# Performance work log

Hardware: AMD Instinct MI355X
Metric: run time of the kernel (lower is better)

## Reference

```python
import jax, jax.numpy as jnp
import numpy as np

N, E, NNZ = 50000, 10000, 250000   # nodes, hyperedges, incidences
IN_CH, H, D = 128, 64, 6           # in_channels, MLP_hidden, stalk dim
EPS = 1e-5


def setup_inputs() -> dict:
    key = jax.random.key(0)
    ks = jax.random.split(key, 12)
    inp = {}
    inp["x"] = jax.random.normal(ks[0], (N, IN_CH), jnp.float32)
    inp["hyperedge_attr"] = jax.random.normal(ks[1], (E, IN_CH), jnp.float32)  # init_hedge='rand'
    inp["node_idx"] = jax.random.randint(ks[2], (NNZ,), 0, N)
    inp["edge_idx"] = jax.random.randint(ks[3], (NNZ,), 0, E)
    inp["node_types"] = jax.random.randint(ks[4], (N,), 0, 3)
    inp["hyperedge_types"] = jax.random.randint(ks[5], (E,), 0, 6)
    s = 1.0 / np.sqrt(IN_CH)
    inp["W_lin"] = jax.random.uniform(ks[6], (IN_CH, H * D), jnp.float32, -s, s)
    inp["b_lin"] = jnp.zeros((H * D,), jnp.float32)
    inp["ln_g"] = jnp.ones((2 * H,), jnp.float32)
    inp["ln_b"] = jnp.zeros((2 * H,), jnp.float32)
    s2 = 1.0 / np.sqrt(2 * H)
    inp["W_sheaf"] = jax.random.uniform(ks[7], (2 * H, D), jnp.float32, -s2, s2)
    inp["b_sheaf"] = jnp.zeros((D,), jnp.float32)
    s3 = 1.0 / np.sqrt(H)
    inp["W_conv0"] = jax.random.uniform(ks[8], (H, H), jnp.float32, -s3, s3)
    inp["b_conv0"] = jnp.zeros((H,), jnp.float32)
    inp["W_conv1"] = jax.random.uniform(ks[9], (H, H), jnp.float32, -s3, s3)
    inp["b_conv1"] = jnp.zeros((H,), jnp.float32)
    return inp


def _layernorm(x, g, b):
    mu = x.mean(-1, keepdims=True)
    var = ((x - mu) ** 2).mean(-1, keepdims=True)
    return (x - mu) * jax.lax.rsqrt(var + EPS) * g + b


def reference(x, hyperedge_attr, node_idx, edge_idx, node_types, hyperedge_types,
              W_lin, b_lin, ln_g, ln_b, W_sheaf, b_sheaf,
              W_conv0, b_conv0, W_conv1, b_conv1):
    # --- input projection + stalk reshape (self.lin) ---
    xs = (x @ W_lin + b_lin).reshape(N * D, H)              # [N*d, H]
    es = (hyperedge_attr @ W_lin + b_lin).reshape(E * D, H)  # [E*d, H]

    # --- SheafBuilderDiag (local_concat, sigmoid act) ---
    xa = xs.reshape(N, D, H).mean(1)   # [N, H] stalk-averaged node feats
    ea = es.reshape(E, D, H).mean(1)   # [E, H]
    feat = jnp.concatenate([xa[node_idx], ea[edge_idx]], axis=-1)  # [NNZ, 2H]
    alpha = jax.nn.sigmoid(_layernorm(feat, ln_g, ln_b) @ W_sheaf + b_sheaf)  # [NNZ, D]

    dr = jnp.arange(D)
    row_exp = (node_idx[:, None] * D + dr).reshape(-1)  # [NNZ*D] expanded node index
    col_exp = (edge_idx[:, None] * D + dr).reshape(-1)  # [NNZ*D] expanded hyperedge index
    a = alpha.reshape(-1)                               # [NNZ*D]

    # --- degree_norm: D^-1 (nodes) and B^-1 (hyperedges) from incidence counts ---
    ones = jnp.ones_like(a)
    Dn = jax.ops.segment_sum(ones, row_exp, num_segments=N * D)
    Dinv = jnp.where(Dn > 0, 1.0 / Dn, 0.0)
    Bn = jax.ops.segment_sum(ones, col_exp, num_segments=E * D)
    Binv = jnp.where(Bn > 0, 1.0 / Bn, 0.0)

    def conv(xin, W, bias):
        # HyperDiffusionDiagSheafConv: out = xW - D^-1 H^T B^-1 H (xW) + bias
        xl = xin @ W
        m = Binv[:, None] * jax.ops.segment_sum(a[:, None] * xl[row_exp], col_exp, num_segments=E * D)
        agg = Dinv[:, None] * jax.ops.segment_sum(a[:, None] * m[col_exp], row_exp, num_segments=N * D)
        return xl - agg + bias

    h1 = jax.nn.elu(conv(xs, W_conv0, b_conv0))   # dropout inactive (eval)
    h2 = conv(h1, W_conv1, b_conv1)
    return jax.nn.elu(h2.reshape(N, H * D))
```

## Files before the change

### kernel.cpp

```cpp
#include <hip/hip_runtime.h>
#include <hip/hip_bf16.h>

#define N_NODES 50000
#define N_EDGES 10000
#define NNZV    250000
#define IN_CH   128
#define HDIM    64
#define DSTALK  6
#define HD      384
#define NROWS   (N_NODES * DSTALK)
#define EROWS   (N_EDGES * DSTALK)

__global__ __launch_bounds__(256) void k_weff(
    const float* __restrict__ W_lin, const float* __restrict__ W0,
    float* __restrict__ W0eff) {
  int idx = blockIdx.x * blockDim.x + threadIdx.x;
  if (idx >= IN_CH * HD) return;
  int k = idx / HD, j = idx - k * HD;
  int r = j >> 6, h = j & 63;
  float s = 0.f;
#pragma unroll 8
  for (int m = 0; m < HDIM; m++)
    s += W_lin[k * HD + r * HDIM + m] * W0[m * HDIM + h];
  W0eff[idx] = s;
}

#define WS_BASE (IN_CH * HDIM + HD + HDIM)
__global__ __launch_bounds__(256) void k_wsmall(
    const float* __restrict__ W_lin, const float* __restrict__ b_lin,
    const float* __restrict__ W0,
    const float* __restrict__ g, const float* __restrict__ bln,
    const float* __restrict__ Ws, const float* __restrict__ bs,
    float* __restrict__ Wm, float* __restrict__ cm, float* __restrict__ c0,
    float* __restrict__ gwN, float* __restrict__ gwE,
    float* __restrict__ G, float* __restrict__ K) {
  int idx = blockIdx.x * blockDim.x + threadIdx.x;
  if (idx < IN_CH * HDIM) {
    int k = idx >> 6, h = idx & 63;
    float s = 0.f;
#pragma unroll
    for (int r = 0; r < DSTALK; r++) s += W_lin[k * HD + r * HDIM + h];
    Wm[idx] = s * (1.f / 6.f);
  } else if (idx < IN_CH * HDIM + HD) {
    int j = idx - IN_CH * HDIM;
    int r = j >> 6, h = j & 63;
    float s = 0.f;
#pragma unroll 8
    for (int m = 0; m < HDIM; m++) s += b_lin[r * HDIM + m] * W0[m * HDIM + h];
    c0[j] = s;
  } else if (idx < WS_BASE) {
    int h = idx - IN_CH * HDIM - HD;
    float s = 0.f;
#pragma unroll
    for (int r = 0; r < DSTALK; r++) s += b_lin[r * HDIM + h];
    cm[h] = s * (1.f / 6.f);
  } else if (idx < WS_BASE + 384) {
    int i = idx - WS_BASE;
    int h = i / 6, r = i - h * 6;
    gwN[i] = g[h] * Ws[h * DSTALK + r];
  } else if (idx < WS_BASE + 768) {
    int i = idx - WS_BASE - 384;
    int h = i / 6, r = i - h * 6;
    gwE[i] = g[64 + h] * Ws[(64 + h) * DSTALK + r];
  } else if (idx < WS_BASE + 774) {
    int r = idx - WS_BASE - 768;
    float s = 0.f;
    for (int i = 0; i < 2 * HDIM; i++) s += g[i] * Ws[i * DSTALK + r];
    G[r] = s;
  } else if (idx < WS_BASE + 780) {
    int r = idx - WS_BASE - 774;
    float s = 0.f;
    for (int i = 0; i < 2 * HDIM; i++) s += bln[i] * Ws[i * DSTALK + r];
    K[r] = s + bs[r];
  }
}

__global__ __launch_bounds__(256) void k_xa_stats(
    const float* __restrict__ x, const float* __restrict__ ea,
    const float* __restrict__ Wm, const float* __restrict__ cm,
    const float* __restrict__ gwN, const float* __restrict__ gwE,
    float* __restrict__ stats) {
  __shared__ float lx[64][IN_CH];
  __shared__ float ox[64][HDIM + 1];
  __shared__ float lgw[2][64 * DSTALK];
  const int row0 = blockIdx.x * 64;
  const int tid = threadIdx.x;
  for (int i = tid; i < 2 * 64 * DSTALK; i += 256) {
    int which = i / 384, k = i - which * 384;
    lgw[which][k] = which ? gwE[k] : gwN[k];
  }
  for (int i = tid; i < 64 * IN_CH; i += 256) {
    int r = i >> 7, k = i & 127;
    int row = row0 + r;
    float v = 0.f;
    if (row < N_NODES) v = x[row * IN_CH + k];
    else if (row < N_NODES + N_EDGES) v = ea[(row - N_NODES) * IN_CH + k];
    lx[r][k] = v;
  }
  __syncthreads();
  const int col = tid & 63, rg = tid >> 6;
  float acc[16];
#pragma unroll
  for (int i = 0; i < 16; i++) acc[i] = 0.f;
  for (int k = 0; k < IN_CH; k++) {
    float w = Wm[k * HDIM + col];
#pragma unroll
    for (int i = 0; i < 16; i++) acc[i] += lx[rg * 16 + i][k] * w;
  }
  const float c = cm[col];
#pragma unroll
  for (int i = 0; i < 16; i++) ox[rg * 16 + i][col] = acc[i] + c;
  __syncthreads();
  for (int t = tid; t < 512; t += 256) {
    int row = t >> 3, st = t & 7;
    int grow = row0 + row;
    if (grow >= N_NODES + N_EDGES) continue;
    const float* __restrict__ gw = (grow >= N_NODES) ? lgw[1] : lgw[0];
    float s = 0.f;
    if (st == 0) {
#pragma unroll 8
      for (int h = 0; h < HDIM; h++) s += ox[row][h];
    } else if (st == 1) {
#pragma unroll 8
      for (int h = 0; h < HDIM; h++) { float v = ox[row][h]; s += v * v; }
    } else {
      int r = st - 2;
#pragma unroll 8
      for (int h = 0; h < HDIM; h++) s += ox[row][h] * gw[h * DSTALK + r];
    }
    stats[(size_t)grow * 8 + st] = s;
  }
}

__global__ __launch_bounds__(384) void k_xl0(
    const float* __restrict__ x, const float* __restrict__ W0eff,
    const float* __restrict__ c0, float* __restrict__ xl0) {
  __shared__ float lx[16][IN_CH];
  const int row0 = blockIdx.x * 16;
  const int tid = threadIdx.x;
  for (int i = tid; i < 16 * IN_CH; i += 384) {
    int r = i >> 7, k = i & 127;
    int row = row0 + r;
    lx[r][k] = (row < N_NODES) ? x[row * IN_CH + k] : 0.f;
  }
  __syncthreads();
  const int j = tid;
  float acc[16];
#pragma unroll
  for (int r = 0; r < 16; r++) acc[r] = 0.f;
  for (int k = 0; k < IN_CH; k++) {
    float w = W0eff[k * HD + j];
#pragma unroll
    for (int r = 0; r < 16; r++) acc[r] += lx[r][k] * w;
  }
  const float bb = c0[j];
#pragma unroll
  for (int r = 0; r < 16; r++) {
    int row = row0 + r;
    if (row < N_NODES) xl0[(size_t)row * HD + j] = acc[r] + bb;
  }
}

__global__ __launch_bounds__(256) void k_sheaf2(
    const int* __restrict__ nidx, const int* __restrict__ eidx,
    const float* __restrict__ stats,
    const float* __restrict__ G, const float* __restrict__ K,
    float* __restrict__ alpha) {
  int j = blockIdx.x * blockDim.x + threadIdx.x;
  if (j >= NNZV) return;
  int n = nidx[j], e = eidx[j];
  const float4* __restrict__ sn = (const float4*)(stats + (size_t)n * 8);
  const float4* __restrict__ se = (const float4*)(stats + ((size_t)(N_NODES + e)) * 8);
  float4 a0 = sn[0], a1 = sn[1];
  float4 b0 = se[0], b1 = se[1];
  float mu = (a0.x + b0.x) * (1.f / 128.f);
  float var = (a0.y + b0.y) * (1.f / 128.f) - mu * mu;
  float rs = rsqrtf(var + 1e-5f);
  float p[DSTALK] = {a0.z + b0.z, a0.w + b0.w, a1.x + b1.x,
                     a1.y + b1.y, a1.z + b1.z, a1.w + b1.w};
#pragma unroll
  for (int r = 0; r < DSTALK; r++) {
    float z = rs * (p[r] - mu * G[r]) + K[r];
    alpha[(size_t)j * DSTALK + r] = 1.f / (1.f + expf(-z));
  }
}

__global__ void k_count(const int* __restrict__ nidx, const int* __restrict__ eidx,
                        int* __restrict__ cntN, int* __restrict__ cntE) {
  int j = blockIdx.x * blockDim.x + threadIdx.x;
  if (j < NNZV) {
    atomicAdd(&cntN[nidx[j]], 1);
    atomicAdd(&cntE[eidx[j]], 1);
  }
}

__global__ __launch_bounds__(256) void k_scan_a(
    const int* __restrict__ cnt, int n, int* __restrict__ row,
    int* __restrict__ bsum) {
  const int b = blockIdx.x, t = threadIdx.x;
  const int i0 = b * 512 + 2 * t, i1 = i0 + 1;
  int c0 = (i0 < n) ? cnt[i0] : 0;
  int c1 = (i1 < n) ? cnt[i1] : 0;
  int ts = c0 + c1;
  const int lane = t & 63, wv = t >> 6;
  int s = ts;
#pragma unroll
  for (int o = 1; o < 64; o <<= 1) {
    int v = __shfl_up(s, o);
    if (lane >= o) s += v;
  }
  __shared__ int wsum[4];
  if (lane == 63) wsum[wv] = s;
  __syncthreads();
  int wbase = 0;
#pragma unroll
  for (int wprev = 0; wprev < 3; wprev++)
    if (wprev < wv) wbase += wsum[wprev];
  const int incl = wbase + s;
  const int excl = incl - ts;
  if (i0 < n) row[i0] = excl;
  if (i1 < n) row[i1] = excl + c0;
  if (t == 255) bsum[b] = incl;
}

__global__ __launch_bounds__(128) void k_scan_b(
    const int* __restrict__ bsum, int nb, int* __restrict__ bbase) {
  const int t = threadIdx.x;
  int v = (t < nb) ? bsum[t] : 0;
  const int lane = t & 63, wv = t >> 6;
  int s = v;
#pragma unroll
  for (int o = 1; o < 64; o <<= 1) {
    int u = __shfl_up(s, o);
    if (lane >= o) s += u;
  }
  __shared__ int wsum[2];
  if (lane == 63) wsum[wv] = s;
  __syncthreads();
  const int incl = ((wv == 1) ? wsum[0] : 0) + s;
  if (t < nb) bbase[t] = incl - v;
  if (t == 127) bbase[nb] = incl;
}

__global__ __launch_bounds__(256) void k_scan_c(
    const int* __restrict__ cnt, const int* __restrict__ bbase, int n, int nb,
    int* __restrict__ row, int* __restrict__ fill, float* __restrict__ inv) {
  int i = blockIdx.x * blockDim.x + threadIdx.x;
  if (i < n) {
    int v = row[i] + bbase[i >> 9];
    row[i] = v;
    fill[i] = v;
    int c = cnt[i];
    inv[i] = c > 0 ? 1.f / (float)c : 0.f;
  }
  if (i == 0) row[n] = bbase[nb];
}

__global__ void k_fill(const int* __restrict__ nidx, const int* __restrict__ eidx,
                       int* __restrict__ fillN, int* __restrict__ fillE,
                       int* __restrict__ jlN, int* __restrict__ jlE) {
  int j = blockIdx.x * blockDim.x + threadIdx.x;
  if (j < NNZV) {
    int p = atomicAdd(&fillN[nidx[j]], 1);
    jlN[p] = j;
    int q = atomicAdd(&fillE[eidx[j]], 1);
    jlE[q] = j;
  }
}

__global__ __launch_bounds__(256) void k_xw(const float* __restrict__ xin,
                                            const float* __restrict__ W,
                                            float* __restrict__ xl) {
  __shared__ float lw[64][64];
  __shared__ float lx[16][64];
  const int tid = threadIdx.x;
  for (int i = tid; i < 64 * 64; i += 256) lw[i >> 6][i & 63] = W[i];
  const int row0 = blockIdx.x * 16;
  for (int i = tid; i < 16 * 64; i += 256)
    lx[i >> 6][i & 63] = xin[(size_t)(row0 + (i >> 6)) * HDIM + (i & 63)];
  __syncthreads();
  const int c = tid & 63, rg = tid >> 6;
  float acc[4];
#pragma unroll
  for (int rr = 0; rr < 4; rr++) acc[rr] = 0.f;
  for (int k = 0; k < 64; k++) {
    float w = lw[k][c];
#pragma unroll
    for (int rr = 0; rr < 4; rr++) acc[rr] += lx[rg * 4 + rr][k] * w;
  }
  __syncthreads();
#pragma unroll
  for (int rr = 0; rr < 4; rr++)
    xl[(size_t)(row0 + rg * 4 + rr) * HDIM + c] = acc[rr];
}

__global__ __launch_bounds__(256) void k_gather_e(
    const int* __restrict__ rowE, const int* __restrict__ jlE,
    const int* __restrict__ nidx, const float* __restrict__ alpha,
    const float* __restrict__ xl, const float* __restrict__ Binv,
    float* __restrict__ msum) {
  int e = (blockIdx.x * blockDim.x + threadIdx.x) >> 6;
  int lane = threadIdx.x & 63;
  if (e >= N_EDGES) return;
  float acc[DSTALK];
#pragma unroll
  for (int r = 0; r < DSTALK; r++) acc[r] = 0.f;
  const int lo = rowE[e], hi = rowE[e + 1];
  for (int p = lo; p < hi; p++) {
    const int j = jlE[p];
    const int n = nidx[j];
    const float* __restrict__ xr = xl + (size_t)n * HD + lane;
    const float* __restrict__ ar = alpha + (size_t)j * DSTALK;
#pragma unroll
    for (int r = 0; r < DSTALK; r++) acc[r] += ar[r] * xr[r * HDIM];
  }
  const float bv = Binv[e];
  float* __restrict__ mr = msum + (size_t)e * HD + lane;
#pragma unroll
  for (int r = 0; r < DSTALK; r++) mr[r * HDIM] = acc[r] * bv;
}

__global__ __launch_bounds__(256) void k_gather_n(
    const int* __restrict__ rowN, const int* __restrict__ jlN,
    const int* __restrict__ eidx, const float* __restrict__ alpha,
    const float* __restrict__ msum, const float* __restrict__ Dinv,
    const float* __restrict__ xl, const float* __restrict__ bias,
    float* __restrict__ outp) {
  int n = (blockIdx.x * blockDim.x + threadIdx.x) >> 6;
  int lane = threadIdx.x & 63;
  if (n >= N_NODES) return;
  float acc[DSTALK];
#pragma unroll
  for (int r = 0; r < DSTALK; r++) acc[r] = 0.f;
  const int lo = rowN[n], hi = rowN[n + 1];
  for (int p = lo; p < hi; p++) {
    const int j = jlN[p];
    const int e = eidx[j];
    const float* __restrict__ mr = msum + (size_t)e * HD + lane;
    const float* __restrict__ ar = alpha + (size_t)j * DSTALK;
#pragma unroll
    for (int r = 0; r < DSTALK; r++) acc[r] += ar[r] * mr[r * HDIM];
  }
  const float dv = Dinv[n];
  const float bb = bias[lane];
  const float* __restrict__ xr = xl + (size_t)n * HD + lane;
  float* __restrict__ orow = outp + (size_t)n * HD + lane;
#pragma unroll
  for (int r = 0; r < DSTALK; r++) {
    float v = xr[r * HDIM] + bb - dv * acc[r];
    orow[r * HDIM] = v > 0.f ? v : expm1f(v);
  }
}

extern "C" void kernel_launch(void* const* d_in, const int* in_sizes, int n_in,
                              void* d_out, int out_size, void* d_ws, size_t ws_size,
                              hipStream_t stream) {
  const float* x    = (const float*)d_in[0];
  const float* hea  = (const float*)d_in[1];
  const int*  nidx  = (const int*)d_in[2];
  const int*  eidx  = (const int*)d_in[3];
  const float* W_lin = (const float*)d_in[6];
  const float* b_lin = (const float*)d_in[7];
  const float* ln_g  = (const float*)d_in[8];
  const float* ln_b  = (const float*)d_in[9];
  const float* W_sh  = (const float*)d_in[10];
  const float* b_sh  = (const float*)d_in[11];
  const float* W_c0  = (const float*)d_in[12];
  const float* b_c0  = (const float*)d_in[13];
  const float* W_c1  = (const float*)d_in[14];
  const float* b_c1  = (const float*)d_in[15];
  float* out = (float*)d_out;

  char* ws = (char*)d_ws;
  size_t off = 0;
  auto alloc = [&](size_t bytes) {
    size_t o = off;
    off = (off + bytes + 255) & ~(size_t)255;
    return o;
  };
  size_t o_xl0   = alloc((size_t)NROWS * HDIM * 4);
  size_t o_msum  = alloc((size_t)EROWS * HDIM * 4);
  size_t o_alpha = alloc((size_t)NNZV * DSTALK * 4);
  size_t o_stats = alloc((size_t)(N_NODES + N_EDGES) * 8 * 4);
  size_t o_jlN   = alloc((size_t)NNZV * 4);
  size_t o_jlE   = alloc((size_t)NNZV * 4);
  size_t o_cntN  = alloc((size_t)N_NODES * 4);
  size_t o_cntE  = alloc((size_t)N_EDGES * 4);
  size_t o_rowN  = alloc((size_t)(N_NODES + 1) * 4);
  size_t o_rowE  = alloc((size_t)(N_EDGES + 1) * 4);
  size_t o_filN  = alloc((size_t)N_NODES * 4);
  size_t o_filE  = alloc((size_t)N_EDGES * 4);
  size_t o_Dinv  = alloc((size_t)N_NODES * 4);
  size_t o_Binv  = alloc((size_t)N_EDGES * 4);
  size_t o_bsN   = alloc((size_t)256 * 4);
  size_t o_bbN   = alloc((size_t)256 * 4);
  size_t o_bsE   = alloc((size_t)256 * 4);
  size_t o_bbE   = alloc((size_t)256 * 4);
  size_t o_Weff  = alloc((size_t)IN_CH * HD * 4);
  size_t o_Wm    = alloc((size_t)IN_CH * HDIM * 4);
  size_t o_cm    = alloc((size_t)HDIM * 4);
  size_t o_c0    = alloc((size_t)HD * 4);
  size_t o_gwN   = alloc((size_t)64 * DSTALK * 4);
  size_t o_gwE   = alloc((size_t)64 * DSTALK * 4);
  size_t o_G     = alloc((size_t)DSTALK * 4);
  size_t o_K     = alloc((size_t)DSTALK * 4);

  float* xl0   = (float*)(ws + o_xl0);
  float* msum  = (float*)(ws + o_msum);
  float* alpha = (float*)(ws + o_alpha);
  float* stats = (float*)(ws + o_stats);
  int*   jlN   = (int*)(ws + o_jlN);
  int*   jlE   = (int*)(ws + o_jlE);
  int*   cntN  = (int*)(ws + o_cntN);
  int*   cntE  = (int*)(ws + o_cntE);
  int*   rowN  = (int*)(ws + o_rowN);
  int*   rowE  = (int*)(ws + o_rowE);
  int*   filN  = (int*)(ws + o_filN);
  int*   filE  = (int*)(ws + o_filE);
  float* Dinv  = (float*)(ws + o_Dinv);
  float* Binv  = (float*)(ws + o_Binv);
  int*   bsN   = (int*)(ws + o_bsN);
  int*   bbN   = (int*)(ws + o_bbN);
  int*   bsE   = (int*)(ws + o_bsE);
  int*   bbE   = (int*)(ws + o_bbE);
  float* W0eff = (float*)(ws + o_Weff);
  float* Wm    = (float*)(ws + o_Wm);
  float* cm    = (float*)(ws + o_cm);
  float* c0    = (float*)(ws + o_c0);
  float* gwN   = (float*)(ws + o_gwN);
  float* gwE   = (float*)(ws + o_gwE);
  float* G     = (float*)(ws + o_G);
  float* K     = (float*)(ws + o_K);

  const int NB_N = (N_NODES + 511) / 512;
  const int NB_E = (N_EDGES + 511) / 512;

  k_weff<<<(IN_CH * HD + 255) / 256, 256, 0, stream>>>(W_lin, W_c0, W0eff);
  k_wsmall<<<(WS_BASE + 780 + 255) / 256, 256, 0, stream>>>(
      W_lin, b_lin, W_c0, ln_g, ln_b, W_sh, b_sh,
      Wm, cm, c0, gwN, gwE, G, K);

  hipMemsetAsync(ws + o_cntN, 0, (size_t)N_NODES * 4, stream);
  hipMemsetAsync(ws + o_cntE, 0, (size_t)N_EDGES * 4, stream);
  k_count<<<(NNZV + 255) / 256, 256, 0, stream>>>(nidx, eidx, cntN, cntE);
  k_scan_a<<<NB_N, 256, 0, stream>>>(cntN, N_NODES, rowN, bsN);
  k_scan_a<<<NB_E, 256, 0, stream>>>(cntE, N_EDGES, rowE, bsE);
  k_scan_b<<<1, 128, 0, stream>>>(bsN, NB_N, bbN);
  k_scan_b<<<1, 128, 0, stream>>>(bsE, NB_E, bbE);
  k_scan_c<<<(N_NODES + 255) / 256, 256, 0, stream>>>(cntN, bbN, N_NODES, NB_N,
                                                      rowN, filN, Dinv);
  k_scan_c<<<(N_EDGES + 255) / 256, 256, 0, stream>>>(cntE, bbE, N_EDGES, NB_E,
                                                      rowE, filE, Binv);
  k_fill<<<(NNZV + 255) / 256, 256, 0, stream>>>(nidx, eidx, filN, filE, jlN, jlE);

  k_xa_stats<<<(N_NODES + N_EDGES + 63) / 64, 256, 0, stream>>>(
      x, hea, Wm, cm, gwN, gwE, stats);

  k_sheaf2<<<(NNZV + 255) / 256, 256, 0, stream>>>(nidx, eidx, stats, G, K, alpha);

  k_xl0<<<N_NODES / 16, 384, 0, stream>>>(x, W0eff, c0, xl0);
  k_gather_e<<<(N_EDGES + 3) / 4, 256, 0, stream>>>(rowE, jlE, nidx, alpha, xl0, Binv, msum);
  k_gather_n<<<(N_NODES + 3) / 4, 256, 0, stream>>>(rowN, jlN, eidx, alpha, msum, Dinv,
                                                    xl0, b_c0, xl0);

  k_xw<<<NROWS / 16, 256, 0, stream>>>(xl0, W_c1, xl0);
  k_gather_e<<<(N_EDGES + 3) / 4, 256, 0, stream>>>(rowE, jlE, nidx, alpha, xl0, Binv, msum);
  k_gather_n<<<(N_NODES + 3) / 4, 256, 0, stream>>>(rowN, jlN, eidx, alpha, msum, Dinv,
                                                    xl0, b_c1, out);

  (void)in_sizes; (void)n_in; (void)out_size; (void)ws_size;
}
```

Measured before the change: 753.9 us.

## Register-tile the dense GEMMs with transposed weights and store neighbor ids in CSR lists

Measured after the change: 673.0 us. -10.7%, faster.

```diff
diff --git a/kernel.cpp b/kernel.cpp
--- a/kernel.cpp
+++ b/kernel.cpp
@@ -11,9 +11,9 @@
 #define NROWS   (N_NODES * DSTALK)
 #define EROWS   (N_EDGES * DSTALK)
 
-__global__ __launch_bounds__(256) void k_weff(
+__global__ __launch_bounds__(256) void k_wefft(
     const float* __restrict__ W_lin, const float* __restrict__ W0,
-    float* __restrict__ W0eff) {
+    float* __restrict__ W0effT) {
   int idx = blockIdx.x * blockDim.x + threadIdx.x;
   if (idx >= IN_CH * HD) return;
   int k = idx / HD, j = idx - k * HD;
@@ -22,18 +22,19 @@
 #pragma unroll 8
   for (int m = 0; m < HDIM; m++)
     s += W_lin[k * HD + r * HDIM + m] * W0[m * HDIM + h];
-  W0eff[idx] = s;
+  W0effT[(size_t)j * IN_CH + k] = s;
 }
 
 #define WS_BASE (IN_CH * HDIM + HD + HDIM)
+#define WS_END  (WS_BASE + 780 + HDIM * HDIM)
 __global__ __launch_bounds__(256) void k_wsmall(
     const float* __restrict__ W_lin, const float* __restrict__ b_lin,
-    const float* __restrict__ W0,
+    const float* __restrict__ W0, const float* __restrict__ W1,
     const float* __restrict__ g, const float* __restrict__ bln,
     const float* __restrict__ Ws, const float* __restrict__ bs,
     float* __restrict__ Wm, float* __restrict__ cm, float* __restrict__ c0,
     float* __restrict__ gwN, float* __restrict__ gwE,
-    float* __restrict__ G, float* __restrict__ K) {
+    float* __restrict__ G, float* __restrict__ K, float* __restrict__ W1T) {
   int idx = blockIdx.x * blockDim.x + threadIdx.x;
   if (idx < IN_CH * HDIM) {
     int k = idx >> 6, h = idx & 63;
@@ -72,6 +73,10 @@
     float s = 0.f;
     for (int i = 0; i < 2 * HDIM; i++) s += bln[i] * Ws[i * DSTALK + r];
     K[r] = s + bs[r];
+  } else if (idx < WS_END) {
+    int i = idx - WS_BASE - 780;
+    int c = i >> 6, k = i & 63;
+    W1T[c * HDIM + k] = W1[k * HDIM + c];
   }
 }
 
@@ -132,32 +137,98 @@
   }
 }
 
-__global__ __launch_bounds__(384) void k_xl0(
-    const float* __restrict__ x, const float* __restrict__ W0eff,
+__global__ __launch_bounds__(256) void k_xl0(
+    const float* __restrict__ x, const float* __restrict__ W0effT,
     const float* __restrict__ c0, float* __restrict__ xl0) {
-  __shared__ float lx[16][IN_CH];
-  const int row0 = blockIdx.x * 16;
+  __shared__ float4 xav[16][65];
+  __shared__ float4 wbv[16][65];
   const int tid = threadIdx.x;
-  for (int i = tid; i < 16 * IN_CH; i += 384) {
-    int r = i >> 7, k = i & 127;
-    int row = row0 + r;
-    lx[r][k] = (row < N_NODES) ? x[row * IN_CH + k] : 0.f;
+  const int row0 = blockIdx.x * 64;
+  const int col0 = blockIdx.y * 64;
+  const int tc = tid & 15, tr = tid >> 4;
+  float acc[4][4] = {{0.f}};
+  for (int kc = 0; kc < 2; kc++) {
+    if (kc) __syncthreads();
+#pragma unroll
+    for (int i = 0; i < 4; i++) {
+      int fidx = tid + i * 256;
+      int row = fidx >> 4, kq = fidx & 15;
+      int gk = kc * 64 + kq * 4;
+      int grow = row0 + row;
+      float4 v = make_float4(0.f, 0.f, 0.f, 0.f);
+      if (grow < N_NODES) v = *(const float4*)(x + (size_t)grow * IN_CH + gk);
+      xav[kq][row] = v;
+      wbv[kq][row] = *(const float4*)(W0effT + (size_t)(col0 + row) * IN_CH + gk);
+    }
+    __syncthreads();
+    for (int kq = 0; kq < 16; kq++) {
+      float4 xa[4], wb[4];
+#pragma unroll
+      for (int i = 0; i < 4; i++) xa[i] = xav[kq][tr + (i << 4)];
+#pragma unroll
+      for (int j = 0; j < 4; j++) wb[j] = wbv[kq][tc + (j << 4)];
+#pragma unroll
+      for (int i = 0; i < 4; i++)
+#pragma unroll
+        for (int j = 0; j < 4; j++)
+          acc[i][j] += xa[i].x * wb[j].x + xa[i].y * wb[j].y +
+                       xa[i].z * wb[j].z + xa[i].w * wb[j].w;
+    }
+  }
+#pragma unroll
+  for (int i = 0; i < 4; i++) {
+    int row = row0 + tr + (i << 4);
+    if (row >= N_NODES) continue;
+#pragma unroll
+    for (int j = 0; j < 4; j++) {
+      int col = col0 + tc + (j << 4);
+      xl0[(size_t)row * HD + col] = acc[i][j] + c0[col];
+    }
+  }
+}
+
+__global__ __launch_bounds__(256) void k_xw(
+    const float* __restrict__ xin, const float* __restrict__ W1T,
+    float* __restrict__ xl) {
+  __shared__ float4 xav[16][65];
+  __shared__ float4 wbv[16][65];
+  const int tid = threadIdx.x;
+  const int row0 = blockIdx.x * 64;
+  const int tc = tid & 15, tr = tid >> 4;
+#pragma unroll
+  for (int i = 0; i < 4; i++) {
+    int fidx = tid + i * 256;
+    int row = fidx >> 4, kq = fidx & 15;
+    int grow = row0 + row;
+    float4 v = make_float4(0.f, 0.f, 0.f, 0.f);
+    if (grow < NROWS) v = *(const float4*)(xin + (size_t)grow * HDIM + kq * 4);
+    xav[kq][row] = v;
+    wbv[kq][row] = *(const float4*)(W1T + row * HDIM + kq * 4);
   }
   __syncthreads();
-  const int j = tid;
-  float acc[16];
-#pragma unroll
-  for (int r = 0; r < 16; r++) acc[r] = 0.f;
-  for (int k = 0; k < IN_CH; k++) {
-    float w = W0eff[k * HD + j];
-#pragma unroll
-    for (int r = 0; r < 16; r++) acc[r] += lx[r][k] * w;
-  }
-  const float bb = c0[j];
-#pragma unroll
-  for (int r = 0; r < 16; r++) {
-    int row = row0 + r;
-    if (row < N_NODES) xl0[(size_t)row * HD + j] = acc[r] + bb;
+  float acc[4][4] = {{0.f}};
+  for (int kq = 0; kq < 16; kq++) {
+    float4 xa[4], wb[4];
+#pragma unroll
+    for (int i = 0; i < 4; i++) xa[i] = xav[kq][tr + (i << 4)];
+#pragma unroll
+    for (int j = 0; j < 4; j++) wb[j] = wbv[kq][tc + (j << 4)];
+#pragma unroll
+    for (int i = 0; i < 4; i++)
+#pragma unroll
+      for (int j = 0; j < 4; j++)
+        acc[i][j] += xa[i].x * wb[j].x + xa[i].y * wb[j].y +
+                     xa[i].z * wb[j].z + xa[i].w * wb[j].w;
+  }
+#pragma unroll
+  for (int i = 0; i < 4; i++) {
+    int row = row0 + tr + (i << 4);
+    if (row >= NROWS) continue;
+#pragma unroll
+    for (int j = 0; j < 4; j++) {
+      int col = tc + (j << 4);
+      xl[(size_t)row * HDIM + col] = acc[i][j];
+    }
   }
 }
 
@@ -258,45 +329,21 @@
 
 __global__ void k_fill(const int* __restrict__ nidx, const int* __restrict__ eidx,
                        int* __restrict__ fillN, int* __restrict__ fillE,
-                       int* __restrict__ jlN, int* __restrict__ jlE) {
+                       int* __restrict__ jlN, int* __restrict__ jlE,
+                       int* __restrict__ elN, int* __restrict__ nlE) {
   int j = blockIdx.x * blockDim.x + threadIdx.x;
   if (j < NNZV) {
-    int p = atomicAdd(&fillN[nidx[j]], 1);
-    jlN[p] = j;
-    int q = atomicAdd(&fillE[eidx[j]], 1);
-    jlE[q] = j;
-  }
-}
-
-__global__ __launch_bounds__(256) void k_xw(const float* __restrict__ xin,
-                                            const float* __restrict__ W,
-                                            float* __restrict__ xl) {
-  __shared__ float lw[64][64];
-  __shared__ float lx[16][64];
-  const int tid = threadIdx.x;
-  for (int i = tid; i < 64 * 64; i += 256) lw[i >> 6][i & 63] = W[i];
-  const int row0 = blockIdx.x * 16;
-  for (int i = tid; i < 16 * 64; i += 256)
-    lx[i >> 6][i & 63] = xin[(size_t)(row0 + (i >> 6)) * HDIM + (i & 63)];
-  __syncthreads();
-  const int c = tid & 63, rg = tid >> 6;
-  float acc[4];
-#pragma unroll
-  for (int rr = 0; rr < 4; rr++) acc[rr] = 0.f;
-  for (int k = 0; k < 64; k++) {
-    float w = lw[k][c];
-#pragma unroll
-    for (int rr = 0; rr < 4; rr++) acc[rr] += lx[rg * 4 + rr][k] * w;
-  }
-  __syncthreads();
-#pragma unroll
-  for (int rr = 0; rr < 4; rr++)
-    xl[(size_t)(row0 + rg * 4 + rr) * HDIM + c] = acc[rr];
+    int n = nidx[j], e = eidx[j];
+    int p = atomicAdd(&fillN[n], 1);
+    jlN[p] = j; elN[p] = e;
+    int q = atomicAdd(&fillE[e], 1);
+    jlE[q] = j; nlE[q] = n;
+  }
 }
 
 __global__ __launch_bounds__(256) void k_gather_e(
     const int* __restrict__ rowE, const int* __restrict__ jlE,
-    const int* __restrict__ nidx, const float* __restrict__ alpha,
+    const int* __restrict__ nlE, const float* __restrict__ alpha,
     const float* __restrict__ xl, const float* __restrict__ Binv,
     float* __restrict__ msum) {
   int e = (blockIdx.x * blockDim.x + threadIdx.x) >> 6;
@@ -308,7 +355,7 @@
   const int lo = rowE[e], hi = rowE[e + 1];
   for (int p = lo; p < hi; p++) {
     const int j = jlE[p];
-    const int n = nidx[j];
+    const int n = nlE[p];
     const float* __restrict__ xr = xl + (size_t)n * HD + lane;
     const float* __restrict__ ar = alpha + (size_t)j * DSTALK;
 #pragma unroll
@@ -322,7 +369,7 @@
 
 __global__ __launch_bounds__(256) void k_gather_n(
     const int* __restrict__ rowN, const int* __restrict__ jlN,
-    const int* __restrict__ eidx, const float* __restrict__ alpha,
+    const int* __restrict__ elN, const float* __restrict__ alpha,
     const float* __restrict__ msum, const float* __restrict__ Dinv,
     const float* __restrict__ xl, const float* __restrict__ bias,
     float* __restrict__ outp) {
@@ -335,7 +382,7 @@
   const int lo = rowN[n], hi = rowN[n + 1];
   for (int p = lo; p < hi; p++) {
     const int j = jlN[p];
-    const int e = eidx[j];
+    const int e = elN[p];
     const float* __restrict__ mr = msum + (size_t)e * HD + lane;
     const float* __restrict__ ar = alpha + (size_t)j * DSTALK;
 #pragma unroll
@@ -384,6 +431,8 @@
   size_t o_stats = alloc((size_t)(N_NODES + N_EDGES) * 8 * 4);
   size_t o_jlN   = alloc((size_t)NNZV * 4);
   size_t o_jlE   = alloc((size_t)NNZV * 4);
+  size_t o_elN   = alloc((size_t)NNZV * 4);
+  size_t o_nlE   = alloc((size_t)NNZV * 4);
   size_t o_cntN  = alloc((size_t)N_NODES * 4);
   size_t o_cntE  = alloc((size_t)N_EDGES * 4);
   size_t o_rowN  = alloc((size_t)(N_NODES + 1) * 4);
@@ -396,7 +445,7 @@
   size_t o_bbN   = alloc((size_t)256 * 4);
   size_t o_bsE   = alloc((size_t)256 * 4);
   size_t o_bbE   = alloc((size_t)256 * 4);
-  size_t o_Weff  = alloc((size_t)IN_CH * HD * 4);
+  size_t o_WeffT = alloc((size_t)IN_CH * HD * 4);
   size_t o_Wm    = alloc((size_t)IN_CH * HDIM * 4);
   size_t o_cm    = alloc((size_t)HDIM * 4);
   size_t o_c0    = alloc((size_t)HD * 4);
@@ -404,41 +453,45 @@
   size_t o_gwE   = alloc((size_t)64 * DSTALK * 4);
   size_t o_G     = alloc((size_t)DSTALK * 4);
   size_t o_K     = alloc((size_t)DSTALK * 4);
-
-  float* xl0   = (float*)(ws + o_xl0);
-  float* msum  = (float*)(ws + o_msum);
-  float* alpha = (float*)(ws + o_alpha);
-  float* stats = (float*)(ws + o_stats);
-  int*   jlN   = (int*)(ws + o_jlN);
-  int*   jlE   = (int*)(ws + o_jlE);
-  int*   cntN  = (int*)(ws + o_cntN);
-  int*   cntE  = (int*)(ws + o_cntE);
-  int*   rowN  = (int*)(ws + o_rowN);
-  int*   rowE  = (int*)(ws + o_rowE);
-  int*   filN  = (int*)(ws + o_filN);
-  int*   filE  = (int*)(ws + o_filE);
-  float* Dinv  = (float*)(ws + o_Dinv);
-  float* Binv  = (float*)(ws + o_Binv);
-  int*   bsN   = (int*)(ws + o_bsN);
-  int*   bbN   = (int*)(ws + o_bbN);
-  int*   bsE   = (int*)(ws + o_bsE);
-  int*   bbE   = (int*)(ws + o_bbE);
-  float* W0eff = (float*)(ws + o_Weff);
-  float* Wm    = (float*)(ws + o_Wm);
-  float* cm    = (float*)(ws + o_cm);
-  float* c0    = (float*)(ws + o_c0);
-  float* gwN   = (float*)(ws + o_gwN);
-  float* gwE   = (float*)(ws + o_gwE);
-  float* G     = (float*)(ws + o_G);
-  float* K     = (float*)(ws + o_K);
+  size_t o_W1T   = alloc((size_t)HDIM * HDIM * 4);
+
+  float* xl0    = (float*)(ws + o_xl0);
+  float* msum   = (float*)(ws + o_msum);
+  float* alpha  = (float*)(ws + o_alpha);
+  float* stats  = (float*)(ws + o_stats);
+  int*   jlN    = (int*)(ws + o_jlN);
+  int*   jlE    = (int*)(ws + o_jlE);
+  int*   elN    = (int*)(ws + o_elN);
+  int*   nlE    = (int*)(ws + o_nlE);
+  int*   cntN   = (int*)(ws + o_cntN);
+  int*   cntE   = (int*)(ws + o_cntE);
+  int*   rowN   = (int*)(ws + o_rowN);
+  int*   rowE   = (int*)(ws + o_rowE);
+  int*   filN   = (int*)(ws + o_filN);
+  int*   filE   = (int*)(ws + o_filE);
+  float* Dinv   = (float*)(ws + o_Dinv);
+  float* Binv   = (float*)(ws + o_Binv);
+  int*   bsN    = (int*)(ws + o_bsN);
+  int*   bbN    = (int*)(ws + o_bbN);
+  int*   bsE    = (int*)(ws + o_bsE);
+  int*   bbE    = (int*)(ws + o_bbE);
+  float* W0effT = (float*)(ws + o_WeffT);
+  float* Wm     = (float*)(ws + o_Wm);
+  float* cm     = (float*)(ws + o_cm);
+  float* c0     = (float*)(ws + o_c0);
+  float* gwN    = (float*)(ws + o_gwN);
+  float* gwE    = (float*)(ws + o_gwE);
+  float* G      = (float*)(ws + o_G);
+  float* K      = (float*)(ws + o_K);
+  float* W1T    = (float*)(ws + o_W1T);
 
   const int NB_N = (N_NODES + 511) / 512;
   const int NB_E = (N_EDGES + 511) / 512;
 
-  k_weff<<<(IN_CH * HD + 255) / 256, 256, 0, stream>>>(W_lin, W_c0, W0eff);
-  k_wsmall<<<(WS_BASE + 780 + 255) / 256, 256, 0, stream>>>(
-      W_lin, b_lin, W_c0, ln_g, ln_b, W_sh, b_sh,
-      Wm, cm, c0, gwN, gwE, G, K);
+  k_wefft<<<(IN_CH * HD + 255) / 256, 256, 0, stream>>>(W_lin, W_c0, W0effT);
+  k_wsmall<<<(WS_END + 255) / 256, 256, 0, stream>>>(
+      W_lin, b_lin, W_c0, W_c1, ln_g, ln_b, W_sh, b_sh,
+      Wm, cm, c0, gwN, gwE, G, K, W1T);
 
   hipMemsetAsync(ws + o_cntN, 0, (size_t)N_NODES * 4, stream);
   hipMemsetAsync(ws + o_cntE, 0, (size_t)N_EDGES * 4, stream);
@@ -451,21 +504,25 @@
                                                       rowN, filN, Dinv);
   k_scan_c<<<(N_EDGES + 255) / 256, 256, 0, stream>>>(cntE, bbE, N_EDGES, NB_E,
                                                       rowE, filE, Binv);
-  k_fill<<<(NNZV + 255) / 256, 256, 0, stream>>>(nidx, eidx, filN, filE, jlN, jlE);
+  k_fill<<<(NNZV + 255) / 256, 256, 0, stream>>>(nidx, eidx, filN, filE,
+                                                 jlN, jlE, elN, nlE);
 
   k_xa_stats<<<(N_NODES + N_EDGES + 63) / 64, 256, 0, stream>>>(
       x, hea, Wm, cm, gwN, gwE, stats);
 
   k_sheaf2<<<(NNZV + 255) / 256, 256, 0, stream>>>(nidx, eidx, stats, G, K, alpha);
 
-  k_xl0<<<N_NODES / 16, 384, 0, stream>>>(x, W0eff, c0, xl0);
-  k_gather_e<<<(N_EDGES + 3) / 4, 256, 0, stream>>>(rowE, jlE, nidx, alpha, xl0, Binv, msum);
-  k_gather_n<<<(N_NODES + 3) / 4, 256, 0, stream>>>(rowN, jlN, eidx, alpha, msum, Dinv,
+  {
+    dim3 g((N_NODES + 63) / 64, HD / 64);
+    k_xl0<<<g, 256, 0, stream>>>(x, W0effT, c0, xl0);
+  }
+  k_gather_e<<<(N_EDGES + 3) / 4, 256, 0, stream>>>(rowE, jlE, nlE, alpha, xl0, Binv, msum);
+  k_gather_n<<<(N_NODES + 3) / 4, 256, 0, stream>>>(rowN, jlN, elN, alpha, msum, Dinv,
                                                     xl0, b_c0, xl0);
 
-  k_xw<<<NROWS / 16, 256, 0, stream>>>(xl0, W_c1, xl0);
-  k_gather_e<<<(N_EDGES + 3) / 4, 256, 0, stream>>>(rowE, jlE, nidx, alpha, xl0, Binv, msum);
-  k_gather_n<<<(N_NODES + 3) / 4, 256, 0, stream>>>(rowN, jlN, eidx, alpha, msum, Dinv,
+  k_xw<<<(NROWS + 63) / 64, 256, 0, stream>>>(xl0, W1T, xl0);
+  k_gather_e<<<(N_EDGES + 3) / 4, 256, 0, stream>>>(rowE, jlE, nlE, alpha, xl0, Binv, msum);
+  k_gather_n<<<(N_NODES + 3) / 4, 256, 0, stream>>>(rowN, jlN, elN, alpha, msum, Dinv,
                                                     xl0, b_c1, out);
 
   (void)in_sizes; (void)n_in; (void)out_size; (void)ws_size;
```
